# Kernel optimization log

Measured on AMD Instinct MI355X. Metric: run time of the kernel, lower is better.

Reference implementation:

```python
import jax, jax.numpy as jnp
import numpy as np

B, I, H, O = 32768, 256, 512, 128
STEPS = 10
SPARSITY = 0.8
LN_EPS = 1e-5


def _layernorm(x, g, b):
    mu = jnp.mean(x, axis=-1, keepdims=True)
    var = jnp.mean(jnp.square(x - mu), axis=-1, keepdims=True)
    return (x - mu) * jax.lax.rsqrt(var + LN_EPS) * g + b


def _liquid_layer(x_in, W_in, W_rec, bias, tau, A, mask, g, b):
    """One LiquidLayer: STEPS semi-implicit ODE steps + per-step LayerNorm."""
    dt = 1.0 / STEPS
    i_input = x_in @ W_in                      # [B, H], constant across steps
    Wr_T = (W_rec * mask).T                    # sparse recurrent weights, [H, H]

    def step(h, _):
        f = jax.nn.sigmoid(i_input + h @ Wr_T + bias)
        h_new = (h + dt * f * A) / (1.0 + dt / tau + dt * f)
        return _layernorm(h_new, g, b), None

    h0 = jnp.zeros_like(i_input)
    h, _ = jax.lax.scan(step, h0, None, length=STEPS)
    return h


def setup_inputs() -> dict:
    key = jax.random.key(0)
    ks = jax.random.split(key, 16)
    inp = {
        "x": jax.random.normal(ks[0], (B, I), jnp.float32),
        "W_in_0": jax.random.normal(ks[1], (I, H), jnp.float32) * 0.1,
        "W_rec_0": jax.random.normal(ks[2], (H, H), jnp.float32) * 0.1,
        "bias_0": jnp.zeros((H,), jnp.float32),
        "tau_0": jnp.ones((H,), jnp.float32),
        "A_0": jnp.ones((H,), jnp.float32),
        "mask_0": (jax.random.uniform(ks[3], (H, H)) > SPARSITY).astype(jnp.float32),
        "ln_g_0": jnp.ones((H,), jnp.float32),
        "ln_b_0": jnp.zeros((H,), jnp.float32),
        "W_in_1": jax.random.normal(ks[4], (H, H), jnp.float32) * 0.1,
        "W_rec_1": jax.random.normal(ks[5], (H, H), jnp.float32) * 0.1,
        "bias_1": jnp.zeros((H,), jnp.float32),
        "tau_1": jnp.ones((H,), jnp.float32),
        "A_1": jnp.ones((H,), jnp.float32),
        "mask_1": (jax.random.uniform(ks[6], (H, H)) > SPARSITY).astype(jnp.float32),
        "ln_g_1": jnp.ones((H,), jnp.float32),
        "ln_b_1": jnp.zeros((H,), jnp.float32),
        "W_in_2": jax.random.normal(ks[7], (H, H), jnp.float32) * 0.1,
        "W_rec_2": jax.random.normal(ks[8], (H, H), jnp.float32) * 0.1,
        "bias_2": jnp.zeros((H,), jnp.float32),
        "tau_2": jnp.ones((H,), jnp.float32),
        "A_2": jnp.ones((H,), jnp.float32),
        "mask_2": (jax.random.uniform(ks[9], (H, H)) > SPARSITY).astype(jnp.float32),
        "ln_g_2": jnp.ones((H,), jnp.float32),
        "ln_b_2": jnp.zeros((H,), jnp.float32),
        "out_W": jax.random.normal(ks[10], (O, H), jnp.float32) * (1.0 / np.sqrt(H)),
        "out_b": jnp.zeros((O,), jnp.float32),
    }
    return inp


def reference(x,
              W_in_0, W_rec_0, bias_0, tau_0, A_0, mask_0, ln_g_0, ln_b_0,
              W_in_1, W_rec_1, bias_1, tau_1, A_1, mask_1, ln_g_1, ln_b_1,
              W_in_2, W_rec_2, bias_2, tau_2, A_2, mask_2, ln_g_2, ln_b_2,
              out_W, out_b):
    h = _liquid_layer(x, W_in_0, W_rec_0, bias_0, tau_0, A_0, mask_0, ln_g_0, ln_b_0)
    h = _liquid_layer(h, W_in_1, W_rec_1, bias_1, tau_1, A_1, mask_1, ln_g_1, ln_b_1)
    h = _liquid_layer(h, W_in_2, W_rec_2, bias_2, tau_2, A_2, mask_2, ln_g_2, ln_b_2)
    return h @ out_W.T + out_b  # output projection of the final (output) layer
```

## Files before the change

### kernel.cpp

```cpp
#include <hip/hip_runtime.h>

#define HDIM   512
#define BROWS  64
#define NTHR   1024
#define LDA    520
#define STLD   17
#define NSTEPS 10
#define DT     0.1f
#define LNEPS  1e-5f

typedef __attribute__((ext_vector_type(8))) short v8s;
typedef __attribute__((ext_vector_type(4))) float v4f;

static __device__ __forceinline__ ushort f2bf(float f) {
  union { float f; unsigned u; } v; v.f = f;
  unsigned r = v.u + 0x7fffu + ((v.u >> 16) & 1u);
  return (ushort)(r >> 16);
}
static __device__ __forceinline__ float bf2f(unsigned hw) {
  union { unsigned u; float f; } v; v.u = hw << 16;
  return v.f;
}
static __device__ __forceinline__ unsigned cvt_pk_bf16(float lo, float hi) {
  unsigned r;
  asm("v_cvt_pk_bf16_f32 %0, %1, %2" : "=v"(r) : "v"(lo), "v"(hi));
  return r;
}
static __device__ __forceinline__ float rowsum16(float x) {
  union { float f; int i; } u, v;
  u.f = x;
  v.i = __builtin_amdgcn_update_dpp(0, u.i, 0x121, 0xf, 0xf, false); u.f += v.f;
  v.i = __builtin_amdgcn_update_dpp(0, u.i, 0x122, 0xf, 0xf, false); u.f += v.f;
  v.i = __builtin_amdgcn_update_dpp(0, u.i, 0x124, 0xf, 0xf, false); u.f += v.f;
  v.i = __builtin_amdgcn_update_dpp(0, u.i, 0x128, 0xf, 0xf, false); u.f += v.f;
  return u.f;
}

__global__ void pack_w(const float* __restrict__ src, const float* __restrict__ msk,
                       ushort* __restrict__ dst, int K, int N, int trans) {
  int nt = N >> 4;
  int tot = (K >> 5) * nt * 64;
  int f = blockIdx.x * blockDim.x + threadIdx.x;
  if (f >= tot) return;
  int flane = f & 63;
  int rest = f >> 6;
  int ctg = rest % nt;
  int kc = rest / nt;
  int n = ctg * 16 + (flane & 15);
  int kb = kc * 32 + ((flane >> 4) & 3) * 8;
  ushort v[8];
#pragma unroll
  for (int j = 0; j < 8; ++j) {
    int k = kb + j;
    float s;
    if (trans) {
      s = src[(size_t)n * K + k];
      if (msk) s *= msk[(size_t)n * K + k];
    } else {
      s = src[(size_t)k * N + n];
    }
    v[j] = f2bf(s);
  }
  uint4 u;
  u.x = (unsigned)v[0] | ((unsigned)v[1] << 16);
  u.y = (unsigned)v[2] | ((unsigned)v[3] << 16);
  u.z = (unsigned)v[4] | ((unsigned)v[5] << 16);
  u.w = (unsigned)v[6] | ((unsigned)v[7] << 16);
  *(uint4*)(dst + (size_t)f * 8) = u;
}

template <int KC, int NT, int NCT, int RT>
static __device__ __forceinline__ void gemm_tiles(const ushort* hb, const ushort* __restrict__ w,
                                                  int wv, int lane, v4f acc[RT][NCT]) {
  const int q = lane >> 4, n = lane & 15;
#pragma unroll
  for (int rt = 0; rt < RT; ++rt)
#pragma unroll
    for (int ct = 0; ct < NCT; ++ct)
      acc[rt][ct] = (v4f){0.f, 0.f, 0.f, 0.f};
#pragma unroll
  for (int kc = 0; kc < KC; ++kc) {
    v8s a[RT];
#pragma unroll
    for (int rt = 0; rt < RT; ++rt)
      a[rt] = *(const v8s*)(hb + (rt * 16 + n) * LDA + kc * 32 + q * 8);
#pragma unroll
    for (int ct = 0; ct < NCT; ++ct) {
      const int ctg = wv * NCT + ct;
      v8s b = *(const v8s*)(w + ((size_t)(kc * NT + ctg) * 64 + lane) * 8);
#pragma unroll
      for (int rt = 0; rt < RT; ++rt)
        acc[rt][ct] = __builtin_amdgcn_mfma_f32_16x16x32_bf16(a[rt], b, acc[rt][ct], 0, 0, 0);
    }
  }
}

struct LayerP {
  const ushort* win;
  const ushort* wrec;
  const float* bias;
  const float* tau;
  const float* Aamp;
  const float* g;
  const float* b;
};
struct KP {
  const float* x;
  LayerP L[3];
  const ushort* wout;
  const float* outb;
  float* out;
};

__global__ __launch_bounds__(NTHR, 4) void liquid_fused(KP P) {
  extern __shared__ char smem[];
  ushort* hb = (ushort*)smem;
  float2* stats = (float2*)(smem + BROWS * LDA * 2);
  float2* stats2 = stats + BROWS * STLD;

  const int tid = threadIdx.x;
  const int wv = tid >> 6;
  const int lane = tid & 63;
  const int q = lane >> 4;
  const int n = lane & 15;
  const int row0 = blockIdx.x * BROWS;
  const int wc0 = wv * 32;

  {
    const float4* x4 = (const float4*)P.x;
#pragma unroll
    for (int i = 0; i < 4; ++i) {
      int fi = i * NTHR + tid;
      int r = fi >> 6;
      int c4 = fi & 63;
      float4 v = x4[(size_t)(row0 + r) * 64 + c4];
      uint2 o;
      o.x = cvt_pk_bf16(v.x, v.y);
      o.y = cvt_pk_bf16(v.z, v.w);
      *(uint2*)(hb + r * LDA + c4 * 4) = o;
    }
  }
  __syncthreads();

  v4f acc[4][2];
  v4f base[4][2];
  unsigned hsp[4][2][2];
  float ac[2], c1[2], gc[2], bc[2];

#pragma unroll 1
  for (int l = 0; l < 3; ++l) {
    const LayerP& L = P.L[l];
#pragma unroll
    for (int ct = 0; ct < 2; ++ct) {
      int col = wc0 + ct * 16 + n;
      ac[ct] = DT * L.Aamp[col];
      c1[ct] = 1.0f + DT / L.tau[col];
      gc[ct] = L.g[col];
      bc[ct] = L.b[col];
    }

    if (l == 0) gemm_tiles<8, 32, 2, 4>(hb, L.win, wv, lane, acc);
    else        gemm_tiles<16, 32, 2, 4>(hb, L.win, wv, lane, acc);
#pragma unroll
    for (int ct = 0; ct < 2; ++ct) {
      float bias = L.bias[wc0 + ct * 16 + n];
#pragma unroll
      for (int rt = 0; rt < 4; ++rt)
#pragma unroll
        for (int r = 0; r < 4; ++r)
          base[rt][ct][r] = acc[rt][ct][r] + bias;
    }

#pragma unroll 1
    for (int s = 0; s < NSTEPS; ++s) {
      if (s > 0) {
        gemm_tiles<16, 32, 2, 4>(hb, L.wrec, wv, lane, acc);
      } else {
#pragma unroll
        for (int rt = 0; rt < 4; ++rt)
#pragma unroll
          for (int ct = 0; ct < 2; ++ct)
            acc[rt][ct] = (v4f){0.f, 0.f, 0.f, 0.f};
      }

#pragma unroll
      for (int rt = 0; rt < 4; ++rt) {
        float ps[4], p2[4];
#pragma unroll
        for (int r = 0; r < 4; ++r) { ps[r] = 0.f; p2[r] = 0.f; }
#pragma unroll
        for (int ct = 0; ct < 2; ++ct)
#pragma unroll
          for (int r = 0; r < 4; ++r) {
            float arg = acc[rt][ct][r] + base[rt][ct][r];
            float fv = __builtin_amdgcn_rcpf(1.0f + __expf(-arg));
            float hold = (s == 0) ? 0.0f
                                  : bf2f((hsp[rt][ct][r >> 1] >> ((r & 1) * 16)) & 0xffffu);
            float hn = (hold + fv * ac[ct]) * __builtin_amdgcn_rcpf(c1[ct] + DT * fv);
            acc[rt][ct][r] = hn;
            ps[r] += hn;
            p2[r] = fmaf(hn, hn, p2[r]);
          }
#pragma unroll
        for (int r = 0; r < 4; ++r) { ps[r] = rowsum16(ps[r]); p2[r] = rowsum16(p2[r]); }
        if (n == 0) {
#pragma unroll
          for (int r = 0; r < 4; ++r)
            stats[(rt * 16 + q * 4 + r) * STLD + wv] = make_float2(ps[r], p2[r]);
        }
      }
      __syncthreads();
      if (tid < BROWS) {
        float S = 0.f, S2 = 0.f;
#pragma unroll
        for (int i = 0; i < 16; ++i) {
          float2 t = stats[tid * STLD + i];
          S += t.x;
          S2 += t.y;
        }
        float mu = S * (1.0f / HDIM);
        float var = fmaf(-mu, mu, S2 * (1.0f / HDIM));
        stats2[tid] = make_float2(mu, __builtin_amdgcn_rsqf(var + LNEPS));
      }
      __syncthreads();

#pragma unroll
      for (int rt = 0; rt < 4; ++rt) {
        float2 st[4];
#pragma unroll
        for (int r = 0; r < 4; ++r)
          st[r] = stats2[rt * 16 + q * 4 + r];
#pragma unroll
        for (int ct = 0; ct < 2; ++ct) {
          float v0 = (acc[rt][ct][0] - st[0].x) * st[0].y * gc[ct] + bc[ct];
          float v1 = (acc[rt][ct][1] - st[1].x) * st[1].y * gc[ct] + bc[ct];
          float v2 = (acc[rt][ct][2] - st[2].x) * st[2].y * gc[ct] + bc[ct];
          float v3 = (acc[rt][ct][3] - st[3].x) * st[3].y * gc[ct] + bc[ct];
          unsigned p01 = cvt_pk_bf16(v0, v1);
          unsigned p23 = cvt_pk_bf16(v2, v3);
          hsp[rt][ct][0] = p01;
          hsp[rt][ct][1] = p23;
          ushort* wp = hb + (rt * 16 + q * 4) * LDA + wc0 + ct * 16 + n;
          wp[0]       = (ushort)p01;
          wp[LDA]     = (ushort)(p01 >> 16);
          wp[2 * LDA] = (ushort)p23;
          wp[3 * LDA] = (ushort)(p23 >> 16);
        }
      }
      __syncthreads();
    }
  }

  {
    const int ctg = wv & 7;
    const int rg = wv >> 3;
    v4f oa[2];
#pragma unroll
    for (int rt = 0; rt < 2; ++rt) oa[rt] = (v4f){0.f, 0.f, 0.f, 0.f};
#pragma unroll
    for (int kc = 0; kc < 16; ++kc) {
      v8s b = *(const v8s*)(P.wout + ((size_t)(kc * 8 + ctg) * 64 + lane) * 8);
#pragma unroll
      for (int rt = 0; rt < 2; ++rt) {
        v8s a = *(const v8s*)(hb + (rg * 32 + rt * 16 + n) * LDA + kc * 32 + q * 8);
        oa[rt] = __builtin_amdgcn_mfma_f32_16x16x32_bf16(a, b, oa[rt], 0, 0, 0);
      }
    }
    int col = ctg * 16 + n;
    float ob = P.outb[col];
#pragma unroll
    for (int rt = 0; rt < 2; ++rt)
#pragma unroll
      for (int r = 0; r < 4; ++r)
        P.out[(size_t)(row0 + rg * 32 + rt * 16 + q * 4 + r) * 128 + col] = oa[rt][r] + ob;
  }
}

extern "C" void kernel_launch(void* const* d_in, const int* in_sizes, int n_in,
                              void* d_out, int out_size, void* d_ws, size_t ws_size,
                              hipStream_t stream) {
  (void)in_sizes; (void)n_in; (void)out_size; (void)ws_size;
  ushort* ws = (ushort*)d_ws;

  const size_t S_WIN0 = 0;
  const size_t S_WIN1 = S_WIN0 + (size_t)8 * 32 * 64 * 8;
  const size_t S_WIN2 = S_WIN1 + (size_t)16 * 32 * 64 * 8;
  const size_t S_REC0 = S_WIN2 + (size_t)16 * 32 * 64 * 8;
  const size_t S_REC1 = S_REC0 + (size_t)16 * 32 * 64 * 8;
  const size_t S_REC2 = S_REC1 + (size_t)16 * 32 * 64 * 8;
  const size_t S_WOUT = S_REC2 + (size_t)16 * 32 * 64 * 8;

  const float* f[27];
  for (int i = 0; i < 27; ++i) f[i] = (const float*)d_in[i];

  dim3 bt(256);
  pack_w<<<dim3(64),  bt, 0, stream>>>(f[1],  nullptr, ws + S_WIN0, 256, 512, 0);
  pack_w<<<dim3(128), bt, 0, stream>>>(f[9],  nullptr, ws + S_WIN1, 512, 512, 0);
  pack_w<<<dim3(128), bt, 0, stream>>>(f[17], nullptr, ws + S_WIN2, 512, 512, 0);
  pack_w<<<dim3(128), bt, 0, stream>>>(f[2],  f[6],    ws + S_REC0, 512, 512, 1);
  pack_w<<<dim3(128), bt, 0, stream>>>(f[10], f[14],   ws + S_REC1, 512, 512, 1);
  pack_w<<<dim3(128), bt, 0, stream>>>(f[18], f[22],   ws + S_REC2, 512, 512, 1);
  pack_w<<<dim3(32),  bt, 0, stream>>>(f[25], nullptr, ws + S_WOUT, 512, 128, 1);

  KP P;
  P.x = f[0];
  const size_t win_off[3] = {S_WIN0, S_WIN1, S_WIN2};
  const size_t rec_off[3] = {S_REC0, S_REC1, S_REC2};
  for (int l = 0; l < 3; ++l) {
    int bi = 1 + 8 * l;
    P.L[l].win = ws + win_off[l];
    P.L[l].wrec = ws + rec_off[l];
    P.L[l].bias = f[bi + 2];
    P.L[l].tau = f[bi + 3];
    P.L[l].Aamp = f[bi + 4];
    P.L[l].g = f[bi + 6];
    P.L[l].b = f[bi + 7];
  }
  P.wout = ws + S_WOUT;
  P.outb = f[26];
  P.out = (float*)d_out;

  const int smem = BROWS * LDA * 2 + BROWS * STLD * 8 + BROWS * 8;
  hipFuncSetAttribute((const void*)liquid_fused,
                      hipFuncAttributeMaxDynamicSharedMemorySize, smem);
  liquid_fused<<<dim3(32768 / BROWS), dim3(NTHR), smem, stream>>>(P);
}
```

Measured before the change: 945.2 us.

## Swap MFMA operands so hidden dim is M, fold -log2e into weights

```diff
diff --git a/kernel.cpp b/kernel.cpp
--- a/kernel.cpp
+++ b/kernel.cpp
@@ -8,6 +8,7 @@
 #define NSTEPS 10
 #define DT     0.1f
 #define LNEPS  1e-5f
+#define NLOG2E -1.4426950408889634f
 
 typedef __attribute__((ext_vector_type(8))) short v8s;
 typedef __attribute__((ext_vector_type(4))) float v4f;
@@ -17,8 +18,8 @@
   unsigned r = v.u + 0x7fffu + ((v.u >> 16) & 1u);
   return (ushort)(r >> 16);
 }
-static __device__ __forceinline__ float bf2f(unsigned hw) {
-  union { unsigned u; float f; } v; v.u = hw << 16;
+static __device__ __forceinline__ float ubf2f(unsigned bits) {
+  union { unsigned u; float f; } v; v.u = bits;
   return v.f;
 }
 static __device__ __forceinline__ unsigned cvt_pk_bf16(float lo, float hi) {
@@ -26,18 +27,16 @@
   asm("v_cvt_pk_bf16_f32 %0, %1, %2" : "=v"(r) : "v"(lo), "v"(hi));
   return r;
 }
-static __device__ __forceinline__ float rowsum16(float x) {
-  union { float f; int i; } u, v;
-  u.f = x;
-  v.i = __builtin_amdgcn_update_dpp(0, u.i, 0x121, 0xf, 0xf, false); u.f += v.f;
-  v.i = __builtin_amdgcn_update_dpp(0, u.i, 0x122, 0xf, 0xf, false); u.f += v.f;
-  v.i = __builtin_amdgcn_update_dpp(0, u.i, 0x124, 0xf, 0xf, false); u.f += v.f;
-  v.i = __builtin_amdgcn_update_dpp(0, u.i, 0x128, 0xf, 0xf, false); u.f += v.f;
-  return u.f;
+static __device__ __forceinline__ float fexp2(float x) {
+#if __has_builtin(__builtin_amdgcn_exp2f)
+  return __builtin_amdgcn_exp2f(x);
+#else
+  float r; asm("v_exp_f32 %0, %1" : "=v"(r) : "v"(x)); return r;
+#endif
 }
 
 __global__ void pack_w(const float* __restrict__ src, const float* __restrict__ msk,
-                       ushort* __restrict__ dst, int K, int N, int trans) {
+                       ushort* __restrict__ dst, int K, int N, int trans, float scale) {
   int nt = N >> 4;
   int tot = (K >> 5) * nt * 64;
   int f = blockIdx.x * blockDim.x + threadIdx.x;
@@ -59,7 +58,7 @@
     } else {
       s = src[(size_t)k * N + n];
     }
-    v[j] = f2bf(s);
+    v[j] = f2bf(s * scale);
   }
   uint4 u;
   u.x = (unsigned)v[0] | ((unsigned)v[1] << 16);
@@ -69,28 +68,25 @@
   *(uint4*)(dst + (size_t)f * 8) = u;
 }
 
-template <int KC, int NT, int NCT, int RT>
-static __device__ __forceinline__ void gemm_tiles(const ushort* hb, const ushort* __restrict__ w,
-                                                  int wv, int lane, v4f acc[RT][NCT]) {
+template <int KC>
+static __device__ __forceinline__ void gemm_swapped(const ushort* hb, const ushort* __restrict__ w,
+                                                    int wv, int lane,
+                                                    const v4f init[2][4], v4f acc[2][4]) {
   const int q = lane >> 4, n = lane & 15;
 #pragma unroll
-  for (int rt = 0; rt < RT; ++rt)
-#pragma unroll
-    for (int ct = 0; ct < NCT; ++ct)
-      acc[rt][ct] = (v4f){0.f, 0.f, 0.f, 0.f};
+  for (int rt = 0; rt < 2; ++rt)
+#pragma unroll
+    for (int ct = 0; ct < 4; ++ct)
+      acc[rt][ct] = init[rt][ct];
 #pragma unroll
   for (int kc = 0; kc < KC; ++kc) {
-    v8s a[RT];
-#pragma unroll
-    for (int rt = 0; rt < RT; ++rt)
-      a[rt] = *(const v8s*)(hb + (rt * 16 + n) * LDA + kc * 32 + q * 8);
-#pragma unroll
-    for (int ct = 0; ct < NCT; ++ct) {
-      const int ctg = wv * NCT + ct;
-      v8s b = *(const v8s*)(w + ((size_t)(kc * NT + ctg) * 64 + lane) * 8);
-#pragma unroll
-      for (int rt = 0; rt < RT; ++rt)
-        acc[rt][ct] = __builtin_amdgcn_mfma_f32_16x16x32_bf16(a[rt], b, acc[rt][ct], 0, 0, 0);
+    v8s a0 = *(const v8s*)(w + ((size_t)(kc * 32 + 2 * wv + 0) * 64 + lane) * 8);
+    v8s a1 = *(const v8s*)(w + ((size_t)(kc * 32 + 2 * wv + 1) * 64 + lane) * 8);
+#pragma unroll
+    for (int ct = 0; ct < 4; ++ct) {
+      v8s b = *(const v8s*)(hb + (ct * 16 + n) * LDA + kc * 32 + q * 8);
+      acc[0][ct] = __builtin_amdgcn_mfma_f32_16x16x32_bf16(a0, b, acc[0][ct], 0, 0, 0);
+      acc[1][ct] = __builtin_amdgcn_mfma_f32_16x16x32_bf16(a1, b, acc[1][ct], 0, 0, 0);
     }
   }
 }
@@ -124,7 +120,7 @@
   const int q = lane >> 4;
   const int n = lane & 15;
   const int row0 = blockIdx.x * BROWS;
-  const int wc0 = wv * 32;
+  const int hB = wv * 32 + q * 4;
 
   {
     const float4* x4 = (const float4*)P.x;
@@ -142,72 +138,94 @@
   }
   __syncthreads();
 
-  v4f acc[4][2];
-  v4f base[4][2];
-  unsigned hsp[4][2][2];
-  float ac[2], c1[2], gc[2], bc[2];
+  v4f acc[2][4];
+  v4f base[2][4];
+  float ac[2][4], c1[2][4], gp[2][4], bp[2][4];
 
 #pragma unroll 1
   for (int l = 0; l < 3; ++l) {
     const LayerP& L = P.L[l];
-#pragma unroll
-    for (int ct = 0; ct < 2; ++ct) {
-      int col = wc0 + ct * 16 + n;
-      ac[ct] = DT * L.Aamp[col];
-      c1[ct] = 1.0f + DT / L.tau[col];
-      gc[ct] = L.g[col];
-      bc[ct] = L.b[col];
-    }
-
-    if (l == 0) gemm_tiles<8, 32, 2, 4>(hb, L.win, wv, lane, acc);
-    else        gemm_tiles<16, 32, 2, 4>(hb, L.win, wv, lane, acc);
-#pragma unroll
-    for (int ct = 0; ct < 2; ++ct) {
-      float bias = L.bias[wc0 + ct * 16 + n];
-#pragma unroll
-      for (int rt = 0; rt < 4; ++rt)
+    float blx[2][4];
+#pragma unroll
+    for (int rt = 0; rt < 2; ++rt)
+#pragma unroll
+      for (int r = 0; r < 4; ++r) {
+        int hc = hB + rt * 16 + r;
+        ac[rt][r] = DT * L.Aamp[hc];
+        c1[rt][r] = 1.0f + DT / L.tau[hc];
+        gp[rt][r] = L.g[hc];
+        bp[rt][r] = L.b[hc];
+        blx[rt][r] = NLOG2E * L.bias[hc];
+      }
+
+    {
+      v4f zin[2][4];
+#pragma unroll
+      for (int rt = 0; rt < 2; ++rt)
+#pragma unroll
+        for (int ct = 0; ct < 4; ++ct)
+          zin[rt][ct] = (v4f){0.f, 0.f, 0.f, 0.f};
+      if (l == 0) gemm_swapped<8>(hb, L.win, wv, lane, zin, acc);
+      else        gemm_swapped<16>(hb, L.win, wv, lane, zin, acc);
+    }
+#pragma unroll
+    for (int rt = 0; rt < 2; ++rt)
+#pragma unroll
+      for (int ct = 0; ct < 4; ++ct)
 #pragma unroll
         for (int r = 0; r < 4; ++r)
-          base[rt][ct][r] = acc[rt][ct][r] + bias;
-    }
+          base[rt][ct][r] = acc[rt][ct][r] + blx[rt][r];
 
 #pragma unroll 1
     for (int s = 0; s < NSTEPS; ++s) {
       if (s > 0) {
-        gemm_tiles<16, 32, 2, 4>(hb, L.wrec, wv, lane, acc);
+        gemm_swapped<16>(hb, L.wrec, wv, lane, base, acc);
       } else {
 #pragma unroll
-        for (int rt = 0; rt < 4; ++rt)
-#pragma unroll
-          for (int ct = 0; ct < 2; ++ct)
-            acc[rt][ct] = (v4f){0.f, 0.f, 0.f, 0.f};
-      }
-
-#pragma unroll
-      for (int rt = 0; rt < 4; ++rt) {
-        float ps[4], p2[4];
-#pragma unroll
-        for (int r = 0; r < 4; ++r) { ps[r] = 0.f; p2[r] = 0.f; }
-#pragma unroll
-        for (int ct = 0; ct < 2; ++ct)
-#pragma unroll
-          for (int r = 0; r < 4; ++r) {
-            float arg = acc[rt][ct][r] + base[rt][ct][r];
-            float fv = __builtin_amdgcn_rcpf(1.0f + __expf(-arg));
-            float hold = (s == 0) ? 0.0f
-                                  : bf2f((hsp[rt][ct][r >> 1] >> ((r & 1) * 16)) & 0xffffu);
-            float hn = (hold + fv * ac[ct]) * __builtin_amdgcn_rcpf(c1[ct] + DT * fv);
-            acc[rt][ct][r] = hn;
-            ps[r] += hn;
-            p2[r] = fmaf(hn, hn, p2[r]);
+        for (int rt = 0; rt < 2; ++rt)
+#pragma unroll
+          for (int ct = 0; ct < 4; ++ct)
+            acc[rt][ct] = base[rt][ct];
+      }
+
+      float ps[4] = {0.f, 0.f, 0.f, 0.f}, p2[4] = {0.f, 0.f, 0.f, 0.f};
+#pragma unroll
+      for (int rt = 0; rt < 2; ++rt)
+#pragma unroll
+        for (int ct = 0; ct < 4; ++ct) {
+          float h0 = 0.f, h1 = 0.f, h2 = 0.f, h3 = 0.f;
+          if (s > 0) {
+            uint2 hv = *(const uint2*)(hb + (ct * 16 + n) * LDA + hB + rt * 16);
+            h0 = ubf2f(hv.x << 16);
+            h1 = ubf2f(hv.x & 0xffff0000u);
+            h2 = ubf2f(hv.y << 16);
+            h3 = ubf2f(hv.y & 0xffff0000u);
           }
-#pragma unroll
-        for (int r = 0; r < 4; ++r) { ps[r] = rowsum16(ps[r]); p2[r] = rowsum16(p2[r]); }
-        if (n == 0) {
-#pragma unroll
-          for (int r = 0; r < 4; ++r)
-            stats[(rt * 16 + q * 4 + r) * STLD + wv] = make_float2(ps[r], p2[r]);
+          float t0 = 1.0f + fexp2(acc[rt][ct][0]);
+          float t1 = 1.0f + fexp2(acc[rt][ct][1]);
+          float t2 = 1.0f + fexp2(acc[rt][ct][2]);
+          float t3 = 1.0f + fexp2(acc[rt][ct][3]);
+          float n0 = fmaf(h0, t0, ac[rt][0]) * __builtin_amdgcn_rcpf(fmaf(c1[rt][0], t0, DT));
+          float n1 = fmaf(h1, t1, ac[rt][1]) * __builtin_amdgcn_rcpf(fmaf(c1[rt][1], t1, DT));
+          float n2 = fmaf(h2, t2, ac[rt][2]) * __builtin_amdgcn_rcpf(fmaf(c1[rt][2], t2, DT));
+          float n3 = fmaf(h3, t3, ac[rt][3]) * __builtin_amdgcn_rcpf(fmaf(c1[rt][3], t3, DT));
+          acc[rt][ct][0] = n0; acc[rt][ct][1] = n1;
+          acc[rt][ct][2] = n2; acc[rt][ct][3] = n3;
+          ps[ct] += (n0 + n1) + (n2 + n3);
+          p2[ct] = fmaf(n0, n0, fmaf(n1, n1, fmaf(n2, n2, fmaf(n3, n3, p2[ct]))));
         }
+
+#pragma unroll
+      for (int ct = 0; ct < 4; ++ct) {
+        ps[ct] += __shfl_xor(ps[ct], 16);
+        ps[ct] += __shfl_xor(ps[ct], 32);
+        p2[ct] += __shfl_xor(p2[ct], 16);
+        p2[ct] += __shfl_xor(p2[ct], 32);
+      }
+      {
+        float wps = (q == 0) ? ps[0] : (q == 1) ? ps[1] : (q == 2) ? ps[2] : ps[3];
+        float wp2 = (q == 0) ? p2[0] : (q == 1) ? p2[1] : (q == 2) ? p2[2] : p2[3];
+        stats[lane * STLD + wv] = make_float2(wps, wp2);
       }
       __syncthreads();
       if (tid < BROWS) {
@@ -220,31 +238,24 @@
         }
         float mu = S * (1.0f / HDIM);
         float var = fmaf(-mu, mu, S2 * (1.0f / HDIM));
-        stats2[tid] = make_float2(mu, __builtin_amdgcn_rsqf(var + LNEPS));
+        float rsig = __builtin_amdgcn_rsqf(var + LNEPS);
+        stats2[tid] = make_float2(-mu * rsig, rsig);
       }
       __syncthreads();
 
 #pragma unroll
-      for (int rt = 0; rt < 4; ++rt) {
-        float2 st[4];
-#pragma unroll
-        for (int r = 0; r < 4; ++r)
-          st[r] = stats2[rt * 16 + q * 4 + r];
-#pragma unroll
-        for (int ct = 0; ct < 2; ++ct) {
-          float v0 = (acc[rt][ct][0] - st[0].x) * st[0].y * gc[ct] + bc[ct];
-          float v1 = (acc[rt][ct][1] - st[1].x) * st[1].y * gc[ct] + bc[ct];
-          float v2 = (acc[rt][ct][2] - st[2].x) * st[2].y * gc[ct] + bc[ct];
-          float v3 = (acc[rt][ct][3] - st[3].x) * st[3].y * gc[ct] + bc[ct];
-          unsigned p01 = cvt_pk_bf16(v0, v1);
-          unsigned p23 = cvt_pk_bf16(v2, v3);
-          hsp[rt][ct][0] = p01;
-          hsp[rt][ct][1] = p23;
-          ushort* wp = hb + (rt * 16 + q * 4) * LDA + wc0 + ct * 16 + n;
-          wp[0]       = (ushort)p01;
-          wp[LDA]     = (ushort)(p01 >> 16);
-          wp[2 * LDA] = (ushort)p23;
-          wp[3 * LDA] = (ushort)(p23 >> 16);
+      for (int ct = 0; ct < 4; ++ct) {
+        float2 st = stats2[ct * 16 + n];
+#pragma unroll
+        for (int rt = 0; rt < 2; ++rt) {
+          float v0 = fmaf(fmaf(acc[rt][ct][0], st.y, st.x), gp[rt][0], bp[rt][0]);
+          float v1 = fmaf(fmaf(acc[rt][ct][1], st.y, st.x), gp[rt][1], bp[rt][1]);
+          float v2 = fmaf(fmaf(acc[rt][ct][2], st.y, st.x), gp[rt][2], bp[rt][2]);
+          float v3 = fmaf(fmaf(acc[rt][ct][3], st.y, st.x), gp[rt][3], bp[rt][3]);
+          uint2 o;
+          o.x = cvt_pk_bf16(v0, v1);
+          o.y = cvt_pk_bf16(v2, v3);
+          *(uint2*)(hb + (ct * 16 + n) * LDA + hB + rt * 16) = o;
         }
       }
       __syncthreads();
@@ -294,13 +305,13 @@
   for (int i = 0; i < 27; ++i) f[i] = (const float*)d_in[i];
 
   dim3 bt(256);
-  pack_w<<<dim3(64),  bt, 0, stream>>>(f[1],  nullptr, ws + S_WIN0, 256, 512, 0);
-  pack_w<<<dim3(128), bt, 0, stream>>>(f[9],  nullptr, ws + S_WIN1, 512, 512, 0);
-  pack_w<<<dim3(128), bt, 0, stream>>>(f[17], nullptr, ws + S_WIN2, 512, 512, 0);
-  pack_w<<<dim3(128), bt, 0, stream>>>(f[2],  f[6],    ws + S_REC0, 512, 512, 1);
-  pack_w<<<dim3(128), bt, 0, stream>>>(f[10], f[14],   ws + S_REC1, 512, 512, 1);
-  pack_w<<<dim3(128), bt, 0, stream>>>(f[18], f[22],   ws + S_REC2, 512, 512, 1);
-  pack_w<<<dim3(32),  bt, 0, stream>>>(f[25], nullptr, ws + S_WOUT, 512, 128, 1);
+  pack_w<<<dim3(64),  bt, 0, stream>>>(f[1],  nullptr, ws + S_WIN0, 256, 512, 0, NLOG2E);
+  pack_w<<<dim3(128), bt, 0, stream>>>(f[9],  nullptr, ws + S_WIN1, 512, 512, 0, NLOG2E);
+  pack_w<<<dim3(128), bt, 0, stream>>>(f[17], nullptr, ws + S_WIN2, 512, 512, 0, NLOG2E);
+  pack_w<<<dim3(128), bt, 0, stream>>>(f[2],  f[6],    ws + S_REC0, 512, 512, 1, NLOG2E);
+  pack_w<<<dim3(128), bt, 0, stream>>>(f[10], f[14],   ws + S_REC1, 512, 512, 1, NLOG2E);
+  pack_w<<<dim3(128), bt, 0, stream>>>(f[18], f[22],   ws + S_REC2, 512, 512, 1, NLOG2E);
+  pack_w<<<dim3(32),  bt, 0, stream>>>(f[25], nullptr, ws + S_WOUT, 512, 128, 1, 1.0f);
 
   KP P;
   P.x = f[0];
```

After: 1.001 ms. 1.06x slower.
